# Kernel optimization log

Measured on AMD Instinct MI355X. Metric: run time of the kernel, lower is better.

## Reference

```python
import jax, jax.numpy as jnp
import numpy as np

B, S, HID = 4, 2048, 1024
NH, HD = 16, 64  # op_heads, head_size (hidden_size // total_heads)
EPS = 1e-6


def setup_inputs() -> dict:
    key = jax.random.key(0)
    k1, k2, k3, k4 = jax.random.split(key, 4)
    return {
        "hidden_states": jax.random.normal(k1, (B, S, HID), dtype=jnp.float32),
        "assoc_hc_attn": jax.random.uniform(k2, (B, S, S), dtype=jnp.float32),
        "broad_hc_attn": jax.random.uniform(k3, (B, S, S), dtype=jnp.float32),
        "Wv": jax.random.normal(k4, (HID, NH * HD), dtype=jnp.float32) * 0.02,
        "bv": jnp.zeros((NH * HD,), dtype=jnp.float32),
    }


def reference(hidden_states, assoc_hc_attn, broad_hc_attn, Wv, bv):
    # v_proj + split heads -> [B, NH, S, HD]
    value = hidden_states @ Wv + bv
    sp_value = value.reshape(B, S, NH, HD).transpose(0, 2, 1, 3)

    # broad_heads == 0, so attn_heads == assoc_hc_attn broadcast over all op_heads.
    attn = assoc_hc_attn.astype(jnp.float32)  # [B, S, S]
    causal = jnp.tril(jnp.ones((S, S), dtype=bool))
    attn = jnp.where(causal, attn, 0.0)
    # sum-normalize along keys (no softmax)
    attn = attn / (EPS + attn.sum(axis=-1, keepdims=True))

    # shared attn across heads: contract once -> [B, NH, S, HD]
    out = jnp.einsum('bqk,bhkd->bhqd', attn, sp_value)
    # merge heads -> [B, S, NH*HD]
    return out.transpose(0, 2, 1, 3).reshape(B, S, NH * HD)
```

## Files before the change

### kernel.cpp

```cpp
#include <hip/hip_runtime.h>

#define B_    4
#define S_    2048
#define HID_  1024
#define NO_   1024
#define EPS_  1e-6f
#define M1_   (B_ * S_)

typedef __attribute__((ext_vector_type(8))) short  short8;
typedef __attribute__((ext_vector_type(4))) float  f32x4;
typedef unsigned short ushort_t;

__device__ __forceinline__ unsigned short f2bf(float f) {
  union { float f; unsigned int u; } v; v.f = f;
  unsigned int r = v.u + 0x7FFFu + ((v.u >> 16) & 1u);
  return (unsigned short)(r >> 16);
}
__device__ __forceinline__ unsigned pack2(float a, float b) {
  return (unsigned)f2bf(a) | ((unsigned)f2bf(b) << 16);
}

typedef __attribute__((address_space(1))) const void GASV;
typedef __attribute__((address_space(3))) void LASV;
__device__ __forceinline__ void gld16(const void* g, void* l) {
  __builtin_amdgcn_global_load_lds((GASV*)g, (LASV*)l, 16, 0, 0);
}

__global__ __launch_bounds__(256) void k_prep(
    const float* __restrict__ Wv, ushort_t* __restrict__ WvT,
    const float* __restrict__ H,  ushort_t* __restrict__ Hb,
    const float* __restrict__ A,  ushort_t* __restrict__ Ab) {
  int id = blockIdx.x;
  if (id < 1024) {
    __shared__ float tile[32][33];
    int k0 = (id & 31) * 32;
    int n0 = (id >> 5) * 32;
    int tx = threadIdx.x & 31, ty = threadIdx.x >> 5;
    for (int i = ty; i < 32; i += 8)
      tile[i][tx] = Wv[(size_t)(k0 + i) * NO_ + n0 + tx];
    __syncthreads();
    for (int i = ty; i < 32; i += 8)
      WvT[(size_t)(n0 + i) * HID_ + k0 + tx] = f2bf(tile[tx][i]);
  } else if (id < 1024 + 8192) {
    size_t i = ((size_t)(id - 1024) * 256 + threadIdx.x) * 4;
    float4 v = *(const float4*)(H + i);
    uint2 p; p.x = pack2(v.x, v.y); p.y = pack2(v.z, v.w);
    *(uint2*)(Hb + i) = p;
  } else {
    int row  = (id - 9216) * 4 + (threadIdx.x >> 6);
    int lane = threadIdx.x & 63;
    int q = row & 2047;
    int wend = ((q >> 7) + 1) << 7;
    const float* rp = A + (size_t)row * S_;
    float4 v[8];
    float s = 0.f;
#pragma unroll
    for (int i = 0; i < 8; i++) {
      int k = i * 256 + lane * 4;
      if (k < wend) {
        float4 t = *(const float4*)(rp + k);
        t.x = (k + 0 <= q) ? t.x : 0.f;
        t.y = (k + 1 <= q) ? t.y : 0.f;
        t.z = (k + 2 <= q) ? t.z : 0.f;
        t.w = (k + 3 <= q) ? t.w : 0.f;
        v[i] = t;
        s += t.x + t.y + t.z + t.w;
      }
    }
    for (int off = 1; off < 64; off <<= 1) s += __shfl_xor(s, off, 64);
    float inv = 1.0f / (EPS_ + s);
    ushort_t* op = Ab + (size_t)row * S_;
#pragma unroll
    for (int i = 0; i < 8; i++) {
      int k = i * 256 + lane * 4;
      if (k < wend) {
        uint2 p;
        p.x = pack2(v[i].x * inv, v[i].y * inv);
        p.y = pack2(v[i].z * inv, v[i].w * inv);
        *(uint2*)(op + k) = p;
      }
    }
  }
}

__global__ __launch_bounds__(256) void k_vt(
    const ushort_t* __restrict__ WvT, const ushort_t* __restrict__ Hb,
    const float* __restrict__ bv, ushort_t* __restrict__ Vt) {
  __shared__ __align__(16) ushort_t lds_a[128 * 32];
  __shared__ __align__(16) ushort_t lds_b[128 * 32];
  int m0 = blockIdx.x * 128;
  int n0 = blockIdx.y * 128;
  int tid = threadIdx.x;
  int wave = tid >> 6, lane = tid & 63;
  int lq = lane >> 4, lm = lane & 15;
  int wr = wave >> 1, wc = wave & 1;

  int rr = lane >> 2;
  int sc = (lane & 3) ^ ((rr >> 1) & 3);
  const ushort_t* gA = WvT + (size_t)(n0 + wave * 32 + rr) * HID_ + sc * 8;
  const ushort_t* gB = Hb  + (size_t)(m0 + wave * 32 + rr) * HID_ + sc * 8;
  char* la = (char*)lds_a;
  char* lb = (char*)lds_b;
  char* la_w = la + wave * 2048;
  char* lb_w = lb + wave * 2048;
  int swz = (lm >> 1) & 3;
  int fo = (lq ^ swz) << 4;

  f32x4 acc[4][4];
  for (int i = 0; i < 4; i++) for (int j = 0; j < 4; j++) acc[i][j] = (f32x4)0.0f;

  for (int it = 0; it < HID_ / 32; it++) {
    gld16(gA,               la_w);
    gld16(gA + 16 * HID_,   la_w + 1024);
    gld16(gB,               lb_w);
    gld16(gB + 16 * HID_,   lb_w + 1024);
    gA += 32; gB += 32;
    __syncthreads();
    short8 af[4], bfr[4];
#pragma unroll
    for (int mi = 0; mi < 4; mi++)
      af[mi] = *(const short8*)(la + (wr * 64 + mi * 16 + lm) * 64 + fo);
#pragma unroll
    for (int ni = 0; ni < 4; ni++)
      bfr[ni] = *(const short8*)(lb + (wc * 64 + ni * 16 + lm) * 64 + fo);
#pragma unroll
    for (int mi = 0; mi < 4; mi++)
#pragma unroll
      for (int ni = 0; ni < 4; ni++)
        acc[mi][ni] = __builtin_amdgcn_mfma_f32_16x16x32_bf16(af[mi], bfr[ni], acc[mi][ni], 0, 0, 0);
    __syncthreads();
  }
  for (int mi = 0; mi < 4; mi++) {
    for (int r = 0; r < 4; r++) {
      int n = n0 + wr * 64 + mi * 16 + lq * 4 + r;
      float bias = bv[n];
      for (int ni = 0; ni < 4; ni++) {
        int m = m0 + wc * 64 + ni * 16 + lm;
        int b = m >> 11;
        int s = m & 2047;
        Vt[((size_t)b * NO_ + n) * S_ + s] = f2bf(acc[mi][ni][r] + bias);
      }
    }
  }
}

__global__ __launch_bounds__(256) void k_attn(
    const ushort_t* __restrict__ Ab, const ushort_t* __restrict__ Vt,
    float* __restrict__ out) {
  __shared__ __align__(16) ushort_t lds_a[128 * 32];
  __shared__ __align__(16) ushort_t lds_b[128 * 32];
  int col = blockIdx.x;
  int n0 = (col & 7) * 128;
  int b  = col >> 3;
  int y  = (int)blockIdx.y;
  int t  = (y < 8) ? (15 - y) : (y - 8);
  int q0 = t * 128;
  int tid = threadIdx.x;
  int wave = tid >> 6, lane = tid & 63;
  int lq = lane >> 4, lm = lane & 15;
  int wr = wave >> 1, wc = wave & 1;

  int rr = lane >> 2;
  int sc = (lane & 3) ^ ((rr >> 1) & 3);
  const ushort_t* gA = Ab + ((size_t)(b * S_ + q0 + wave * 32 + rr)) * S_ + sc * 8;
  const ushort_t* gB = Vt + ((size_t)(b * NO_ + n0 + wave * 32 + rr)) * S_ + sc * 8;
  char* la = (char*)lds_a;
  char* lb = (char*)lds_b;
  char* la_w = la + wave * 2048;
  char* lb_w = lb + wave * 2048;
  int swz = (lm >> 1) & 3;
  int fo = (lq ^ swz) << 4;

  f32x4 acc[4][4];
  for (int i = 0; i < 4; i++) for (int j = 0; j < 4; j++) acc[i][j] = (f32x4)0.0f;

  const int iters = 4 * t + 4;
  for (int it = 0; it < iters; it++) {
    gld16(gA,             la_w);
    gld16(gA + 16 * S_,   la_w + 1024);
    gld16(gB,             lb_w);
    gld16(gB + 16 * S_,   lb_w + 1024);
    gA += 32; gB += 32;
    __syncthreads();
    short8 af[4], bfr[4];
#pragma unroll
    for (int mi = 0; mi < 4; mi++)
      af[mi] = *(const short8*)(la + (wr * 64 + mi * 16 + lm) * 64 + fo);
#pragma unroll
    for (int ni = 0; ni < 4; ni++)
      bfr[ni] = *(const short8*)(lb + (wc * 64 + ni * 16 + lm) * 64 + fo);
#pragma unroll
    for (int mi = 0; mi < 4; mi++)
#pragma unroll
      for (int ni = 0; ni < 4; ni++)
        acc[mi][ni] = __builtin_amdgcn_mfma_f32_16x16x32_bf16(af[mi], bfr[ni], acc[mi][ni], 0, 0, 0);
    __syncthreads();
  }
  for (int mi = 0; mi < 4; mi++) {
    for (int r = 0; r < 4; r++) {
      int q = q0 + wr * 64 + mi * 16 + lq * 4 + r;
      for (int ni = 0; ni < 4; ni++) {
        int n = n0 + wc * 64 + ni * 16 + lm;
        out[((size_t)(b * S_ + q)) * NO_ + n] = acc[mi][ni][r];
      }
    }
  }
}

extern "C" void kernel_launch(void* const* d_in, const int* in_sizes, int n_in,
                              void* d_out, int out_size, void* d_ws, size_t ws_size,
                              hipStream_t stream) {
  const float* H  = (const float*)d_in[0];
  const float* A  = (const float*)d_in[1];
  const float* Wv = (const float*)d_in[3];
  const float* bv = (const float*)d_in[4];
  float* out = (float*)d_out;

  char* ws = (char*)d_ws;
  ushort_t* WvT = (ushort_t*)ws;
  ushort_t* Hb  = (ushort_t*)(ws + 2097152);
  ushort_t* Vt  = (ushort_t*)(ws + 2097152 + 16777216);
  ushort_t* Abf = (ushort_t*)(ws + 2097152 + 2 * 16777216);

  k_prep <<<1024 + 8192 + 2048, 256, 0, stream>>>(Wv, WvT, H, Hb, A, Abf);
  k_vt   <<<dim3(M1_ / 128, NO_ / 128), 256, 0, stream>>>(WvT, Hb, bv, Vt);
  k_attn <<<dim3(32, 16), 256, 0, stream>>>(Abf, Vt, out);
}
```

Before: 238.4 us.

## Add 4-stage LDS prefetch pipeline and pair causal tiles per block

Both GEMM kernels now use a four-buffer LDS ring filled by async global_load_lds three tiles ahead, with explicit vmcnt waits and raw barriers replacing the load-then-syncthreads pattern, so memory latency overlaps MFMA work. The attention kernel also launches half as many blocks, each handling a short causal row tile and its complementary long one (t and 15-t), which balances work across blocks. This quadruples LDS use, which may lower occupancy, and relies on hand-counted vmcnt values being correct.

```diff
diff --git a/kernel.cpp b/kernel.cpp
--- a/kernel.cpp
+++ b/kernel.cpp
@@ -86,8 +86,8 @@
 __global__ __launch_bounds__(256) void k_vt(
     const ushort_t* __restrict__ WvT, const ushort_t* __restrict__ Hb,
     const float* __restrict__ bv, ushort_t* __restrict__ Vt) {
-  __shared__ __align__(16) ushort_t lds_a[128 * 32];
-  __shared__ __align__(16) ushort_t lds_b[128 * 32];
+  __shared__ __align__(16) ushort_t lds_a[4 * 128 * 32];
+  __shared__ __align__(16) ushort_t lds_b[4 * 128 * 32];
   int m0 = blockIdx.x * 128;
   int n0 = blockIdx.y * 128;
   int tid = threadIdx.x;
@@ -97,8 +97,8 @@
 
   int rr = lane >> 2;
   int sc = (lane & 3) ^ ((rr >> 1) & 3);
-  const ushort_t* gA = WvT + (size_t)(n0 + wave * 32 + rr) * HID_ + sc * 8;
-  const ushort_t* gB = Hb  + (size_t)(m0 + wave * 32 + rr) * HID_ + sc * 8;
+  const ushort_t* pa = WvT + (size_t)(n0 + wave * 32 + rr) * HID_ + sc * 8;
+  const ushort_t* pb = Hb  + (size_t)(m0 + wave * 32 + rr) * HID_ + sc * 8;
   char* la = (char*)lds_a;
   char* lb = (char*)lds_b;
   char* la_w = la + wave * 2048;
@@ -106,29 +106,44 @@
   int swz = (lm >> 1) & 3;
   int fo = (lq ^ swz) << 4;
 
+  auto STAGE = [&](int tile) {
+    char* da = la_w + (tile & 3) * 8192;
+    char* db = lb_w + (tile & 3) * 8192;
+    gld16(pa,             da);
+    gld16(pa + 16 * HID_, da + 1024);
+    gld16(pb,             db);
+    gld16(pb + 16 * HID_, db + 1024);
+    pa += 32; pb += 32;
+  };
+
   f32x4 acc[4][4];
   for (int i = 0; i < 4; i++) for (int j = 0; j < 4; j++) acc[i][j] = (f32x4)0.0f;
 
-  for (int it = 0; it < HID_ / 32; it++) {
-    gld16(gA,               la_w);
-    gld16(gA + 16 * HID_,   la_w + 1024);
-    gld16(gB,               lb_w);
-    gld16(gB + 16 * HID_,   lb_w + 1024);
-    gA += 32; gB += 32;
-    __syncthreads();
+  const int iters = HID_ / 32;
+  STAGE(0); STAGE(1); STAGE(2);
+  for (int it = 0; it < iters; ++it) {
+    int rem = iters - 1 - it;
+    if (rem >= 3) { STAGE(it + 3); asm volatile("s_waitcnt vmcnt(12)" ::: "memory"); }
+    else if (rem == 2) { asm volatile("s_waitcnt vmcnt(8)"  ::: "memory"); }
+    else if (rem == 1) { asm volatile("s_waitcnt vmcnt(4)"  ::: "memory"); }
+    else               { asm volatile("s_waitcnt vmcnt(0)"  ::: "memory"); }
+    __builtin_amdgcn_s_barrier();
+    const char* ra = la + (it & 3) * 8192;
+    const char* rb = lb + (it & 3) * 8192;
     short8 af[4], bfr[4];
 #pragma unroll
     for (int mi = 0; mi < 4; mi++)
-      af[mi] = *(const short8*)(la + (wr * 64 + mi * 16 + lm) * 64 + fo);
+      af[mi] = *(const short8*)(ra + (wr * 64 + mi * 16 + lm) * 64 + fo);
 #pragma unroll
     for (int ni = 0; ni < 4; ni++)
-      bfr[ni] = *(const short8*)(lb + (wc * 64 + ni * 16 + lm) * 64 + fo);
+      bfr[ni] = *(const short8*)(rb + (wc * 64 + ni * 16 + lm) * 64 + fo);
 #pragma unroll
     for (int mi = 0; mi < 4; mi++)
 #pragma unroll
       for (int ni = 0; ni < 4; ni++)
         acc[mi][ni] = __builtin_amdgcn_mfma_f32_16x16x32_bf16(af[mi], bfr[ni], acc[mi][ni], 0, 0, 0);
-    __syncthreads();
+    asm volatile("" ::: "memory");
+    __builtin_amdgcn_s_barrier();
   }
   for (int mi = 0; mi < 4; mi++) {
     for (int r = 0; r < 4; r++) {
@@ -147,14 +162,11 @@
 __global__ __launch_bounds__(256) void k_attn(
     const ushort_t* __restrict__ Ab, const ushort_t* __restrict__ Vt,
     float* __restrict__ out) {
-  __shared__ __align__(16) ushort_t lds_a[128 * 32];
-  __shared__ __align__(16) ushort_t lds_b[128 * 32];
+  __shared__ __align__(16) ushort_t lds_a[4 * 128 * 32];
+  __shared__ __align__(16) ushort_t lds_b[4 * 128 * 32];
   int col = blockIdx.x;
   int n0 = (col & 7) * 128;
   int b  = col >> 3;
-  int y  = (int)blockIdx.y;
-  int t  = (y < 8) ? (15 - y) : (y - 8);
-  int q0 = t * 128;
   int tid = threadIdx.x;
   int wave = tid >> 6, lane = tid & 63;
   int lq = lane >> 4, lm = lane & 15;
@@ -162,8 +174,6 @@
 
   int rr = lane >> 2;
   int sc = (lane & 3) ^ ((rr >> 1) & 3);
-  const ushort_t* gA = Ab + ((size_t)(b * S_ + q0 + wave * 32 + rr)) * S_ + sc * 8;
-  const ushort_t* gB = Vt + ((size_t)(b * NO_ + n0 + wave * 32 + rr)) * S_ + sc * 8;
   char* la = (char*)lds_a;
   char* lb = (char*)lds_b;
   char* la_w = la + wave * 2048;
@@ -171,39 +181,63 @@
   int swz = (lm >> 1) & 3;
   int fo = (lq ^ swz) << 4;
 
-  f32x4 acc[4][4];
-  for (int i = 0; i < 4; i++) for (int j = 0; j < 4; j++) acc[i][j] = (f32x4)0.0f;
-
-  const int iters = 4 * t + 4;
-  for (int it = 0; it < iters; it++) {
-    gld16(gA,             la_w);
-    gld16(gA + 16 * S_,   la_w + 1024);
-    gld16(gB,             lb_w);
-    gld16(gB + 16 * S_,   lb_w + 1024);
-    gA += 32; gB += 32;
-    __syncthreads();
-    short8 af[4], bfr[4];
-#pragma unroll
-    for (int mi = 0; mi < 4; mi++)
-      af[mi] = *(const short8*)(la + (wr * 64 + mi * 16 + lm) * 64 + fo);
-#pragma unroll
-    for (int ni = 0; ni < 4; ni++)
-      bfr[ni] = *(const short8*)(lb + (wc * 64 + ni * 16 + lm) * 64 + fo);
-#pragma unroll
-    for (int mi = 0; mi < 4; mi++)
+  const ushort_t* gB0 = Vt + ((size_t)(b * NO_ + n0 + wave * 32 + rr)) * S_ + sc * 8;
+
+  for (int seg = 0; seg < 2; ++seg) {
+    int t  = (seg == 0) ? (int)blockIdx.y : (15 - (int)blockIdx.y);
+    int q0 = t * 128;
+    const int iters = 4 * t + 4;
+    const ushort_t* pa = Ab + ((size_t)(b * S_ + q0 + wave * 32 + rr)) * S_ + sc * 8;
+    const ushort_t* pb = gB0;
+
+    auto STAGE = [&](int tile) {
+      char* da = la_w + (tile & 3) * 8192;
+      char* db = lb_w + (tile & 3) * 8192;
+      gld16(pa,           da);
+      gld16(pa + 16 * S_, da + 1024);
+      gld16(pb,           db);
+      gld16(pb + 16 * S_, db + 1024);
+      pa += 32; pb += 32;
+    };
+
+    f32x4 acc[4][4];
+    for (int i = 0; i < 4; i++) for (int j = 0; j < 4; j++) acc[i][j] = (f32x4)0.0f;
+
+    STAGE(0); STAGE(1); STAGE(2);
+    for (int it = 0; it < iters; ++it) {
+      int rem = iters - 1 - it;
+      if (rem >= 3) { STAGE(it + 3); asm volatile("s_waitcnt vmcnt(12)" ::: "memory"); }
+      else if (rem == 2) { asm volatile("s_waitcnt vmcnt(8)"  ::: "memory"); }
+      else if (rem == 1) { asm volatile("s_waitcnt vmcnt(4)"  ::: "memory"); }
+      else               { asm volatile("s_waitcnt vmcnt(0)"  ::: "memory"); }
+      __builtin_amdgcn_s_barrier();
+      const char* ra = la + (it & 3) * 8192;
+      const char* rb = lb + (it & 3) * 8192;
+      short8 af[4], bfr[4];
+#pragma unroll
+      for (int mi = 0; mi < 4; mi++)
+        af[mi] = *(const short8*)(ra + (wr * 64 + mi * 16 + lm) * 64 + fo);
 #pragma unroll
       for (int ni = 0; ni < 4; ni++)
-        acc[mi][ni] = __builtin_amdgcn_mfma_f32_16x16x32_bf16(af[mi], bfr[ni], acc[mi][ni], 0, 0, 0);
-    __syncthreads();
-  }
-  for (int mi = 0; mi < 4; mi++) {
-    for (int r = 0; r < 4; r++) {
-      int q = q0 + wr * 64 + mi * 16 + lq * 4 + r;
-      for (int ni = 0; ni < 4; ni++) {
-        int n = n0 + wc * 64 + ni * 16 + lm;
-        out[((size_t)(b * S_ + q)) * NO_ + n] = acc[mi][ni][r];
-      }
-    }
+        bfr[ni] = *(const short8*)(rb + (wc * 64 + ni * 16 + lm) * 64 + fo);
+#pragma unroll
+      for (int mi = 0; mi < 4; mi++)
+#pragma unroll
+        for (int ni = 0; ni < 4; ni++)
+          acc[mi][ni] = __builtin_amdgcn_mfma_f32_16x16x32_bf16(af[mi], bfr[ni], acc[mi][ni], 0, 0, 0);
+      asm volatile("" ::: "memory");
+      __builtin_amdgcn_s_barrier();
+    }
+    for (int mi = 0; mi < 4; mi++) {
+      for (int r = 0; r < 4; r++) {
+        int q = q0 + wr * 64 + mi * 16 + lq * 4 + r;
+        for (int ni = 0; ni < 4; ni++) {
+          int n = n0 + wc * 64 + ni * 16 + lm;
+          out[((size_t)(b * S_ + q)) * NO_ + n] = acc[mi][ni][r];
+        }
+      }
+    }
+    asm volatile("s_waitcnt vmcnt(0)" ::: "memory");
   }
 }
 
@@ -224,5 +258,5 @@
 
   k_prep <<<1024 + 8192 + 2048, 256, 0, stream>>>(Wv, WvT, H, Hb, A, Abf);
   k_vt   <<<dim3(M1_ / 128, NO_ / 128), 256, 0, stream>>>(WvT, Hb, bv, Vt);
-  k_attn <<<dim3(32, 16), 256, 0, stream>>>(Abf, Vt, out);
-}
+  k_attn <<<dim3(32, 8), 256, 0, stream>>>(Abf, Vt, out);
+}
```

Result: no change. 235.0 us (-1.5%).

## Pipeline GEMMs with triple-buffered LDS, 512-thread blocks, XCD-aware tiling, paired causal tiles

Applied to the files above, without the earlier changes.

Both GEMM kernels move to 512-thread blocks with a triple-buffered LDS pipeline: global-to-LDS loads are issued two K-steps ahead, completion is gated with explicit vmcnt waits and raw barriers, and the MFMA sections run at raised wave priority. Block indices are remapped so each XCD works on related tiles, improving L2 reuse. In the attention kernel each block now handles one short and one long causal query tile (t and 15-t), which evens out per-block work across the triangular mask. The cost is more LDS per block and hand-tuned waitcnt logic that must stay exactly right to avoid races.

```diff
diff --git a/kernel.cpp b/kernel.cpp
--- a/kernel.cpp
+++ b/kernel.cpp
@@ -83,59 +83,92 @@
   }
 }
 
-__global__ __launch_bounds__(256) void k_vt(
+__global__ __launch_bounds__(512) void k_vt(
     const ushort_t* __restrict__ WvT, const ushort_t* __restrict__ Hb,
     const float* __restrict__ bv, ushort_t* __restrict__ Vt) {
-  __shared__ __align__(16) ushort_t lds_a[128 * 32];
-  __shared__ __align__(16) ushort_t lds_b[128 * 32];
-  int m0 = blockIdx.x * 128;
-  int n0 = blockIdx.y * 128;
+  __shared__ __align__(16) char lds[3 * 32768];
+  int id  = blockIdx.x;
+  int xcd = id & 7;
+  int mem = id >> 3;
+  int n0  = (mem & 7) * 128;
+  int m0  = (xcd * 8 + (mem >> 3)) * 128;
   int tid = threadIdx.x;
   int wave = tid >> 6, lane = tid & 63;
   int lq = lane >> 4, lm = lane & 15;
-  int wr = wave >> 1, wc = wave & 1;
+  int wq = wave >> 2, wn = wave & 3;
 
   int rr = lane >> 2;
   int sc = (lane & 3) ^ ((rr >> 1) & 3);
-  const ushort_t* gA = WvT + (size_t)(n0 + wave * 32 + rr) * HID_ + sc * 8;
-  const ushort_t* gB = Hb  + (size_t)(m0 + wave * 32 + rr) * HID_ + sc * 8;
-  char* la = (char*)lds_a;
-  char* lb = (char*)lds_b;
-  char* la_w = la + wave * 2048;
-  char* lb_w = lb + wave * 2048;
-  int swz = (lm >> 1) & 3;
-  int fo = (lq ^ swz) << 4;
-
-  f32x4 acc[4][4];
-  for (int i = 0; i < 4; i++) for (int j = 0; j < 4; j++) acc[i][j] = (f32x4)0.0f;
-
-  for (int it = 0; it < HID_ / 32; it++) {
-    gld16(gA,               la_w);
-    gld16(gA + 16 * HID_,   la_w + 1024);
-    gld16(gB,               lb_w);
-    gld16(gB + 16 * HID_,   lb_w + 1024);
-    gA += 32; gB += 32;
-    __syncthreads();
-    short8 af[4], bfr[4];
+  int fo = (lq ^ ((lm >> 1) & 3)) << 4;
+  const ushort_t* pa = WvT + (size_t)(n0 + wave * 16 + rr) * HID_ + sc * 8;
+  const ushort_t* pb = Hb  + (size_t)(m0 + wave * 16 + rr) * HID_ + sc * 8;
+
+  f32x4 acc[4][2];
+  for (int i = 0; i < 4; i++) for (int j = 0; j < 2; j++) acc[i][j] = (f32x4)0.0f;
+
+  const int N = 16;
+
+#pragma unroll
+  for (int tpre = 0; tpre < 2; ++tpre) {
+    char* wb = lds + tpre * 32768;
+    gld16(pa,      wb + wave * 1024);
+    gld16(pa + 32, wb + 8192  + wave * 1024);
+    gld16(pb,      wb + 16384 + wave * 1024);
+    gld16(pb + 32, wb + 24576 + wave * 1024);
+    pa += 64; pb += 64;
+  }
+  asm volatile("s_waitcnt vmcnt(4)" ::: "memory");
+  __builtin_amdgcn_s_barrier();
+
+  int rbuf = 0;
+  for (int it = 0; it < N; ++it) {
+    int wbuf = rbuf + 2; if (wbuf >= 3) wbuf -= 3;
+    bool stg = (it + 2) < N;
+    const char* ra = lds + rbuf * 32768;
+    char* wb = lds + wbuf * 32768;
+    short8 af[4], bf0, bf1;
 #pragma unroll
     for (int mi = 0; mi < 4; mi++)
-      af[mi] = *(const short8*)(la + (wr * 64 + mi * 16 + lm) * 64 + fo);
-#pragma unroll
-    for (int ni = 0; ni < 4; ni++)
-      bfr[ni] = *(const short8*)(lb + (wc * 64 + ni * 16 + lm) * 64 + fo);
+      af[mi] = *(const short8*)(ra + (wq * 64 + mi * 16 + lm) * 64 + fo);
+    bf0 = *(const short8*)(ra + 16384 + (wn * 32 +  0 + lm) * 64 + fo);
+    bf1 = *(const short8*)(ra + 16384 + (wn * 32 + 16 + lm) * 64 + fo);
+    if (stg) { gld16(pa, wb + wave * 1024); gld16(pb, wb + 16384 + wave * 1024); }
+    __builtin_amdgcn_s_barrier();
+    __builtin_amdgcn_s_setprio(1);
+#pragma unroll
+    for (int mi = 0; mi < 4; mi++) {
+      acc[mi][0] = __builtin_amdgcn_mfma_f32_16x16x32_bf16(af[mi], bf0, acc[mi][0], 0, 0, 0);
+      acc[mi][1] = __builtin_amdgcn_mfma_f32_16x16x32_bf16(af[mi], bf1, acc[mi][1], 0, 0, 0);
+    }
+    __builtin_amdgcn_s_setprio(0);
+    __builtin_amdgcn_s_barrier();
 #pragma unroll
     for (int mi = 0; mi < 4; mi++)
-#pragma unroll
-      for (int ni = 0; ni < 4; ni++)
-        acc[mi][ni] = __builtin_amdgcn_mfma_f32_16x16x32_bf16(af[mi], bfr[ni], acc[mi][ni], 0, 0, 0);
-    __syncthreads();
+      af[mi] = *(const short8*)(ra + 8192 + (wq * 64 + mi * 16 + lm) * 64 + fo);
+    bf0 = *(const short8*)(ra + 24576 + (wn * 32 +  0 + lm) * 64 + fo);
+    bf1 = *(const short8*)(ra + 24576 + (wn * 32 + 16 + lm) * 64 + fo);
+    if (stg) { gld16(pa + 32, wb + 8192 + wave * 1024); gld16(pb + 32, wb + 24576 + wave * 1024); pa += 64; pb += 64; }
+    __builtin_amdgcn_s_barrier();
+    __builtin_amdgcn_s_setprio(1);
+#pragma unroll
+    for (int mi = 0; mi < 4; mi++) {
+      acc[mi][0] = __builtin_amdgcn_mfma_f32_16x16x32_bf16(af[mi], bf0, acc[mi][0], 0, 0, 0);
+      acc[mi][1] = __builtin_amdgcn_mfma_f32_16x16x32_bf16(af[mi], bf1, acc[mi][1], 0, 0, 0);
+    }
+    __builtin_amdgcn_s_setprio(0);
+    if (it < N - 1) {
+      if (it + 2 < N) asm volatile("s_waitcnt vmcnt(4)" ::: "memory");
+      else            asm volatile("s_waitcnt vmcnt(0)" ::: "memory");
+    }
+    __builtin_amdgcn_s_barrier();
+    rbuf = (rbuf == 2) ? 0 : rbuf + 1;
   }
   for (int mi = 0; mi < 4; mi++) {
     for (int r = 0; r < 4; r++) {
-      int n = n0 + wr * 64 + mi * 16 + lq * 4 + r;
+      int n = n0 + wq * 64 + mi * 16 + lq * 4 + r;
       float bias = bv[n];
-      for (int ni = 0; ni < 4; ni++) {
-        int m = m0 + wc * 64 + ni * 16 + lm;
+      for (int ni = 0; ni < 2; ni++) {
+        int m = m0 + wn * 32 + ni * 16 + lm;
         int b = m >> 11;
         int s = m & 2047;
         Vt[((size_t)b * NO_ + n) * S_ + s] = f2bf(acc[mi][ni][r] + bias);
@@ -144,66 +177,102 @@
   }
 }
 
-__global__ __launch_bounds__(256) void k_attn(
+__global__ __launch_bounds__(512) void k_attn(
     const ushort_t* __restrict__ Ab, const ushort_t* __restrict__ Vt,
     float* __restrict__ out) {
-  __shared__ __align__(16) ushort_t lds_a[128 * 32];
-  __shared__ __align__(16) ushort_t lds_b[128 * 32];
-  int col = blockIdx.x;
-  int n0 = (col & 7) * 128;
-  int b  = col >> 3;
-  int y  = (int)blockIdx.y;
-  int t  = (y < 8) ? (15 - y) : (y - 8);
-  int q0 = t * 128;
+  __shared__ __align__(16) char lds[3 * 32768];
+  int id  = blockIdx.x;
+  int xcd = id & 7;
+  int mem = id >> 3;
+  int b   = xcd >> 1;
+  int n0  = ((xcd & 1) * 4 + (mem & 3)) * 128;
+  int y   = mem >> 2;
   int tid = threadIdx.x;
   int wave = tid >> 6, lane = tid & 63;
   int lq = lane >> 4, lm = lane & 15;
-  int wr = wave >> 1, wc = wave & 1;
+  int wq = wave >> 2, wn = wave & 3;
 
   int rr = lane >> 2;
   int sc = (lane & 3) ^ ((rr >> 1) & 3);
-  const ushort_t* gA = Ab + ((size_t)(b * S_ + q0 + wave * 32 + rr)) * S_ + sc * 8;
-  const ushort_t* gB = Vt + ((size_t)(b * NO_ + n0 + wave * 32 + rr)) * S_ + sc * 8;
-  char* la = (char*)lds_a;
-  char* lb = (char*)lds_b;
-  char* la_w = la + wave * 2048;
-  char* lb_w = lb + wave * 2048;
-  int swz = (lm >> 1) & 3;
-  int fo = (lq ^ swz) << 4;
-
-  f32x4 acc[4][4];
-  for (int i = 0; i < 4; i++) for (int j = 0; j < 4; j++) acc[i][j] = (f32x4)0.0f;
-
-  const int iters = 4 * t + 4;
-  for (int it = 0; it < iters; it++) {
-    gld16(gA,             la_w);
-    gld16(gA + 16 * S_,   la_w + 1024);
-    gld16(gB,             lb_w);
-    gld16(gB + 16 * S_,   lb_w + 1024);
-    gA += 32; gB += 32;
-    __syncthreads();
-    short8 af[4], bfr[4];
-#pragma unroll
-    for (int mi = 0; mi < 4; mi++)
-      af[mi] = *(const short8*)(la + (wr * 64 + mi * 16 + lm) * 64 + fo);
-#pragma unroll
-    for (int ni = 0; ni < 4; ni++)
-      bfr[ni] = *(const short8*)(lb + (wc * 64 + ni * 16 + lm) * 64 + fo);
-#pragma unroll
-    for (int mi = 0; mi < 4; mi++)
-#pragma unroll
-      for (int ni = 0; ni < 4; ni++)
-        acc[mi][ni] = __builtin_amdgcn_mfma_f32_16x16x32_bf16(af[mi], bfr[ni], acc[mi][ni], 0, 0, 0);
-    __syncthreads();
-  }
-  for (int mi = 0; mi < 4; mi++) {
-    for (int r = 0; r < 4; r++) {
-      int q = q0 + wr * 64 + mi * 16 + lq * 4 + r;
-      for (int ni = 0; ni < 4; ni++) {
-        int n = n0 + wc * 64 + ni * 16 + lm;
-        out[((size_t)(b * S_ + q)) * NO_ + n] = acc[mi][ni][r];
-      }
-    }
+  int fo = (lq ^ ((lm >> 1) & 3)) << 4;
+  const ushort_t* pb0 = Vt + (size_t)(b * NO_ + n0 + wave * 16 + rr) * S_ + sc * 8;
+
+  for (int seg = 0; seg < 2; ++seg) {
+    int t  = seg ? (15 - y) : y;
+    int q0 = t * 128;
+    const int N = 2 * (t + 1);
+    const ushort_t* pa = Ab + (size_t)(b * S_ + q0 + wave * 16 + rr) * S_ + sc * 8;
+    const ushort_t* pb = pb0;
+
+    f32x4 acc[4][2];
+    for (int i = 0; i < 4; i++) for (int j = 0; j < 2; j++) acc[i][j] = (f32x4)0.0f;
+
+#pragma unroll
+    for (int tpre = 0; tpre < 2; ++tpre) {
+      char* wb = lds + tpre * 32768;
+      gld16(pa,      wb + wave * 1024);
+      gld16(pa + 32, wb + 8192  + wave * 1024);
+      gld16(pb,      wb + 16384 + wave * 1024);
+      gld16(pb + 32, wb + 24576 + wave * 1024);
+      pa += 64; pb += 64;
+    }
+    asm volatile("s_waitcnt vmcnt(4)" ::: "memory");
+    __builtin_amdgcn_s_barrier();
+
+    int rbuf = 0;
+    for (int it = 0; it < N; ++it) {
+      int wbuf = rbuf + 2; if (wbuf >= 3) wbuf -= 3;
+      bool stg = (it + 2) < N;
+      const char* ra = lds + rbuf * 32768;
+      char* wb = lds + wbuf * 32768;
+      short8 af[4], bf0, bf1;
+#pragma unroll
+      for (int mi = 0; mi < 4; mi++)
+        af[mi] = *(const short8*)(ra + (wq * 64 + mi * 16 + lm) * 64 + fo);
+      bf0 = *(const short8*)(ra + 16384 + (wn * 32 +  0 + lm) * 64 + fo);
+      bf1 = *(const short8*)(ra + 16384 + (wn * 32 + 16 + lm) * 64 + fo);
+      if (stg) { gld16(pa, wb + wave * 1024); gld16(pb, wb + 16384 + wave * 1024); }
+      __builtin_amdgcn_s_barrier();
+      __builtin_amdgcn_s_setprio(1);
+#pragma unroll
+      for (int mi = 0; mi < 4; mi++) {
+        acc[mi][0] = __builtin_amdgcn_mfma_f32_16x16x32_bf16(af[mi], bf0, acc[mi][0], 0, 0, 0);
+        acc[mi][1] = __builtin_amdgcn_mfma_f32_16x16x32_bf16(af[mi], bf1, acc[mi][1], 0, 0, 0);
+      }
+      __builtin_amdgcn_s_setprio(0);
+      __builtin_amdgcn_s_barrier();
+#pragma unroll
+      for (int mi = 0; mi < 4; mi++)
+        af[mi] = *(const short8*)(ra + 8192 + (wq * 64 + mi * 16 + lm) * 64 + fo);
+      bf0 = *(const short8*)(ra + 24576 + (wn * 32 +  0 + lm) * 64 + fo);
+      bf1 = *(const short8*)(ra + 24576 + (wn * 32 + 16 + lm) * 64 + fo);
+      if (stg) { gld16(pa + 32, wb + 8192 + wave * 1024); gld16(pb + 32, wb + 24576 + wave * 1024); pa += 64; pb += 64; }
+      __builtin_amdgcn_s_barrier();
+      __builtin_amdgcn_s_setprio(1);
+#pragma unroll
+      for (int mi = 0; mi < 4; mi++) {
+        acc[mi][0] = __builtin_amdgcn_mfma_f32_16x16x32_bf16(af[mi], bf0, acc[mi][0], 0, 0, 0);
+        acc[mi][1] = __builtin_amdgcn_mfma_f32_16x16x32_bf16(af[mi], bf1, acc[mi][1], 0, 0, 0);
+      }
+      __builtin_amdgcn_s_setprio(0);
+      if (it < N - 1) {
+        if (it + 2 < N) asm volatile("s_waitcnt vmcnt(4)" ::: "memory");
+        else            asm volatile("s_waitcnt vmcnt(0)" ::: "memory");
+      }
+      __builtin_amdgcn_s_barrier();
+      rbuf = (rbuf == 2) ? 0 : rbuf + 1;
+    }
+    for (int mi = 0; mi < 4; mi++) {
+      for (int r = 0; r < 4; r++) {
+        int q = q0 + wq * 64 + mi * 16 + lq * 4 + r;
+        for (int ni = 0; ni < 2; ni++) {
+          int n = n0 + wn * 32 + ni * 16 + lm;
+          out[((size_t)(b * S_ + q)) * NO_ + n] = acc[mi][ni][r];
+        }
+      }
+    }
+    asm volatile("s_waitcnt vmcnt(0)" ::: "memory");
+    __builtin_amdgcn_s_barrier();
   }
 }
 
@@ -223,6 +292,6 @@
   ushort_t* Abf = (ushort_t*)(ws + 2097152 + 2 * 16777216);
 
   k_prep <<<1024 + 8192 + 2048, 256, 0, stream>>>(Wv, WvT, H, Hb, A, Abf);
-  k_vt   <<<dim3(M1_ / 128, NO_ / 128), 256, 0, stream>>>(WvT, Hb, bv, Vt);
-  k_attn <<<dim3(32, 16), 256, 0, stream>>>(Abf, Vt, out);
-}
+  k_vt   <<<512, 512, 0, stream>>>(WvT, Hb, bv, Vt);
+  k_attn <<<256, 512, 0, stream>>>(Abf, Vt, out);
+}
```

Result: faster. 214.3 us (-10.1%).
